# Performance work log

Hardware: AMD Instinct MI355X
Metric: run time of the kernel (lower is better)

The kernel has to match this reference:

```python
import jax, jax.numpy as jnp
import numpy as np

B, T, N, DIM = 8, 12, 500, 64
N_MIX, N_LAYERS, N_HEADS, N_REL, NG, K = 2, 2, 4, 8, 2, 20


def setup_inputs() -> dict:
    key = jax.random.key(0)
    ks = jax.random.split(key, 9)
    x0 = jax.random.normal(ks[0], (B, DIM, N, T), jnp.float32)
    x1 = jax.random.normal(ks[1], (B, DIM, N, T), jnp.float32)
    # dense relation adjacencies; scaled by 1/N to keep activations numerically sane
    graphs = jax.random.uniform(ks[2], (NG, N, N), jnp.float32) / N
    neighbors = jax.random.randint(ks[3], (NG, N, K), 0, N)
    neighbors_weight = jax.random.uniform(ks[4], (NG, N, K), jnp.float32)
    a_weight = jax.random.normal(ks[5], (2, N_REL, N_HEADS, N_LAYERS, 1, 1), jnp.float32)
    B_weight = jax.random.normal(ks[6], (1, N_HEADS, N_LAYERS, DIM, DIM), jnp.float32) / np.sqrt(DIM).astype(np.float32)
    a_bias = jax.random.normal(ks[7], (2, N_REL, N_HEADS, N_LAYERS, 1), jnp.float32)
    B_bias = jax.random.normal(ks[8], (1, N_HEADS, N_LAYERS, DIM), jnp.float32)
    return {"x0": x0, "x1": x1, "graphs": graphs, "neighbors": neighbors,
            "neighbors_weight": neighbors_weight, "a_weight": a_weight,
            "B_weight": B_weight, "a_bias": a_bias, "B_bias": B_bias}


def _forward(x0, x1, graphs, neighbors, neighbors_weight, a_weight, B_weight, a_bias, B_bias):
    # fuse head-mixture parameters: [R, L, D, D] and [R, L, D]
    wc = jnp.sum(a_weight[0] * B_weight, axis=1)
    bc = jnp.sum(a_bias[0] * B_bias, axis=1)
    wd = jnp.sum(a_weight[1] * B_weight, axis=1)
    bd = jnp.sum(a_bias[1] * B_bias, axis=1)

    xs = [jnp.transpose(x, (0, 3, 2, 1)) for x in (x0, x1)]  # [B, T, N, D]
    g = [[x0], [x1]]  # snapshots in [B, D, N, T] layout
    n_mix = N_MIX
    for l in range(N_LAYERS):
        h = [0.0] * n_mix
        for i in range(n_mix):
            for t in range(NG):
                adj = graphs[t]
                for j in range(n_mix):
                    rel = (t * n_mix + i) * n_mix + j
                    # neighbor aggregation: out[b,t,m,d] = sum_n x[b,t,n,d] * adj[n,m]
                    c = jnp.einsum('btnd,nm->btmd', xs[j], adj)
                    d = jnp.einsum('btnd,nm->btmd', xs[j] - xs[i], adj)
                    c = jax.nn.relu(c @ wc[rel, l] + bc[rel, l])
                    d = jnp.tanh(d @ wd[rel, l] + bd[rel, l])
                    h[i] = h[i] + c + d
        xs = h
        for i in range(n_mix):
            g[i].append(jnp.transpose(xs[i], (0, 3, 2, 1)))
    g = [jnp.concatenate(gi, axis=1) for gi in g]  # [B, D*(L+1), N, T]

    # summarize: per-node neighbor gather + weighted sum, per relation graph
    out = []
    for i in range(n_mix):
        parts = []
        for t in range(NG):
            gathered = g[i][:, :, neighbors[t], :]  # [B, C, N, K, T]
            parts.append(jnp.einsum('bcnkt,nk->bcnt', gathered, neighbors_weight[t]))
        out.append(jnp.concatenate(parts, axis=1))  # [B, C*NG, N, T]
    return tuple(out)


def reference(x0, x1, graphs, neighbors, neighbors_weight, a_weight, B_weight, a_bias, B_bias):
    return _forward(x0, x1, graphs, neighbors, neighbors_weight, a_weight, B_weight, a_bias, B_bias)
```

## Files before the change

### kernel.cpp

```cpp
#include <hip/hip_runtime.h>
#include <hip/hip_bf16.h>
#include <math.h>

#define B_ 8
#define T_ 12
#define N_ 500
#define D_ 64
#define K_ 20
#define M_ (B_*T_)
#define MND_ 3072000

#define XSB_OFF 0ul
#define AGH_OFF (3ul*MND_)
#define AT_HI_OFF (5ul*MND_)
#define XT_OFF    (AT_HI_OFF + 262144ul)
#define WCT_OFF   (XT_OFF + 3145728ul)
#define WDT_OFF   (WCT_OFF + 32768ul)
#define BC_OFF    (WDT_OFF + 32768ul)
#define BD_OFF    (BC_OFF + 1024ul)

using f4 = __attribute__((ext_vector_type(4))) float;
typedef __attribute__((ext_vector_type(8))) short bf16x8;
typedef __attribute__((ext_vector_type(8))) short short8;
typedef __attribute__((ext_vector_type(4))) float f32x4;

__device__ inline ushort to_bf16u(float v) {
    __hip_bfloat16 b = __float2bfloat16(v);
    return *reinterpret_cast<ushort*>(&b);
}

__device__ inline float fast_tanh(float x) {
    float u = __expf(2.0f * x);
    return 1.0f - 2.0f * __builtin_amdgcn_rcpf(u + 1.0f);
}

__global__ __launch_bounds__(256) void fuse_weights(
        const float* __restrict__ aw, const float* __restrict__ Bw,
        const float* __restrict__ ab, const float* __restrict__ Bb,
        float* __restrict__ bc, float* __restrict__ bd,
        ushort* __restrict__ wct, ushort* __restrict__ wdt) {
    int e = blockIdx.x * 256 + threadIdx.x;
    if (e < 131072) {
        int dd = e & 4095; int l = (e >> 12) & 1; int r = (e >> 13) & 7; int cd = e >> 16;
        float s = 0.f;
        #pragma unroll
        for (int h = 0; h < 4; ++h)
            s += aw[((cd*8 + r)*4 + h)*2 + l] * Bw[(h*2 + l)*4096 + dd];
        int tidx = (r*2 + l)*4096 + (dd & 63)*64 + (dd >> 6);
        (cd ? wdt : wct)[tidx] = to_bf16u(s);
    } else {
        int e2 = e - 131072;
        if (e2 < 2048) {
            int d = e2 & 63; int l = (e2 >> 6) & 1; int r = (e2 >> 7) & 7; int cd = e2 >> 10;
            float s = 0.f;
            #pragma unroll
            for (int h = 0; h < 4; ++h)
                s += ab[((cd*8 + r)*4 + h)*2 + l] * Bb[(h*2 + l)*64 + d];
            (cd ? bd : bc)[(r*2 + l)*64 + d] = s;
        }
    }
}

__global__ __launch_bounds__(256) void transpose_in(
        const float* __restrict__ x0, const float* __restrict__ x1,
        ushort* __restrict__ xsb0) {
    int bid = blockIdx.x;
    int n = bid % N_; int b = (bid / N_) % B_; int i = bid / (N_ * B_);
    const float* __restrict__ x = i ? x1 : x0;
    ushort* __restrict__ xbo = xsb0 + (size_t)i * MND_;
    __shared__ float tile[64][13];
    #pragma unroll
    for (int q = 0; q < 3; ++q) {
        int e = q * 256 + threadIdx.x;
        int d = e / 12, t = e % 12;
        tile[d][t] = x[(((size_t)b * D_ + d) * N_ + n) * T_ + t];
    }
    __syncthreads();
    #pragma unroll
    for (int q = 0; q < 3; ++q) {
        int e = q * 256 + threadIdx.x;
        int t = e >> 6, d = e & 63;
        xbo[(((size_t)b * T_ + t) * N_ + n) * D_ + d] = to_bf16u(tile[d][t]);
    }
}

__global__ __launch_bounds__(256) void adj_prep(
        const float* __restrict__ graphs,
        ushort* __restrict__ AT_hi) {
    int t = blockIdx.z;
    int n0 = blockIdx.x * 32, mm0 = blockIdx.y * 32;
    __shared__ float tile[32][33];
    int cc = threadIdx.x & 31, rr = threadIdx.x >> 5;
    #pragma unroll
    for (int it = 0; it < 4; ++it) {
        int n = n0 + it * 8 + rr, mm = mm0 + cc;
        tile[it * 8 + rr][cc] = (n < N_ && mm < N_)
            ? graphs[(size_t)t * 250000 + (size_t)n * 500 + mm] : 0.f;
    }
    __syncthreads();
    #pragma unroll
    for (int it = 0; it < 4; ++it) {
        int mml = it * 8 + rr, nl = cc;
        size_t idx = (size_t)t * 262144 + (size_t)(mm0 + mml) * 512 + n0 + nl;
        AT_hi[idx] = to_bf16u(tile[nl][mml]);
    }
}

__global__ __launch_bounds__(256) void xt_cast(
        const ushort* __restrict__ xsb,
        ushort* __restrict__ XT) {
    int i = blockIdx.z, m = blockIdx.y, c = blockIdx.x;
    int n0 = c * 64;
    __shared__ ushort tile[64][65];
    int d = threadIdx.x & 63, r4 = threadIdx.x >> 6;
    const ushort* __restrict__ src = xsb + (size_t)i * MND_ + (size_t)m * 32000;
    #pragma unroll
    for (int it = 0; it < 16; ++it) {
        int nl = it * 4 + r4; int n = n0 + nl;
        tile[nl][d] = (n < N_) ? src[(size_t)n * 64 + d] : (ushort)0;
    }
    __syncthreads();
    size_t base = (size_t)(i * 96 + m) * 64 * 512 + n0;
    int dl = threadIdx.x >> 2, ng = threadIdx.x & 3;
    #pragma unroll
    for (int half = 0; half < 2; ++half) {
        int nlb = ng * 16 + half * 8;
        short8 hv;
        #pragma unroll
        for (int q = 0; q < 8; ++q) hv[q] = (short)tile[nlb + q][dl];
        *(short8*)(XT + base + (size_t)dl * 512 + nlb) = hv;
    }
}

__global__ __launch_bounds__(64) void aggregate_mfma(
        const ushort* __restrict__ AT_hi,
        const ushort* __restrict__ XT, ushort* __restrict__ aggh) {
    int w = (blockIdx.x & 7) * 384 + (blockIdx.x >> 3);
    const int mm0 = (w & 7) * 64;
    int g = w >> 3;
    const int m = g % 96;
    const int cmb = g / 96;
    const int t = cmb >> 1, j = cmb & 1;
    const int lane = threadIdx.x;
    const int lr = lane & 15;
    const int lk = (lane >> 4) * 8;

    const ushort* __restrict__ A_h = AT_hi + (size_t)t * 262144 + (size_t)(mm0 + lr) * 512 + lk;
    const ushort* __restrict__ Bx  = XT + ((size_t)(j * 96 + m) * 64 + lr) * 512 + lk;

    f32x4 acc[4][4] = {};

    for (int k0 = 0; k0 < 512; k0 += 32) {
        bf16x8 ah[4], bh[4];
        #pragma unroll
        for (int f = 0; f < 4; ++f) {
            ah[f] = *(const bf16x8*)(A_h + (size_t)f * 8192 + k0);
            bh[f] = *(const bf16x8*)(Bx  + (size_t)f * 8192 + k0);
        }
        #pragma unroll
        for (int fi = 0; fi < 4; ++fi)
            #pragma unroll
            for (int fj = 0; fj < 4; ++fj)
                acc[fi][fj] = __builtin_amdgcn_mfma_f32_16x16x32_bf16(ah[fi], bh[fj], acc[fi][fj], 0, 0, 0);
    }

    size_t obase = (size_t)cmb * MND_ + (size_t)m * 32000;
    #pragma unroll
    for (int fi = 0; fi < 4; ++fi) {
        #pragma unroll
        for (int reg = 0; reg < 4; ++reg) {
            int row = mm0 + fi * 16 + (lane >> 4) * 4 + reg;
            if (row < N_) {
                #pragma unroll
                for (int fj = 0; fj < 4; ++fj)
                    aggh[obase + (size_t)row * 64 + fj * 16 + lr] = to_bf16u(acc[fi][fj][reg]);
            }
        }
    }
}

__global__ __launch_bounds__(64) void combine_mfma(
        const ushort* __restrict__ aggh,
        const ushort* __restrict__ wct, const ushort* __restrict__ wdt,
        const float* __restrict__ bcv, const float* __restrict__ bdv,
        ushort* __restrict__ xsb_out,
        ushort* __restrict__ xt_out, int l, int write_xt) {
    const int tile = blockIdx.x;
    const int m = blockIdx.y;
    const int i = blockIdx.z;
    const int n0 = tile * 32;
    const int r0 = m * 500 + n0;
    const int lane = threadIdx.x;
    const int lr = lane & 15;
    const int lk = (lane >> 4) * 8;

    f32x4 hacc[2][4] = {};

    for (int t = 0; t < 2; ++t) {
        #pragma unroll
        for (int j = 0; j < 2; ++j) {
            const int rel = (t * 2 + i) * 2 + j;
            const int wb = (rel * 2 + l) * 4096;
            const ushort* __restrict__ Ajh = aggh + (size_t)(t * 2 + j) * MND_ + (size_t)(r0 + lr) * 64 + lk;
            const ushort* __restrict__ Wc = wct + wb + lr * 64 + lk;

            f32x4 cacc[2][4];
            #pragma unroll
            for (int fj = 0; fj < 4; ++fj) {
                float bv = bcv[(rel * 2 + l) * 64 + fj * 16 + lr];
                #pragma unroll
                for (int fi = 0; fi < 2; ++fi) cacc[fi][fj] = f32x4{bv, bv, bv, bv};
            }

            if (j != i) {
                const ushort* __restrict__ Aih = aggh + (size_t)(t * 2 + i) * MND_ + (size_t)(r0 + lr) * 64 + lk;
                const ushort* __restrict__ Wd = wdt + wb + lr * 64 + lk;
                f32x4 dacc[2][4];
                #pragma unroll
                for (int fj = 0; fj < 4; ++fj) {
                    float bv = bdv[(rel * 2 + l) * 64 + fj * 16 + lr];
                    #pragma unroll
                    for (int fi = 0; fi < 2; ++fi) dacc[fi][fj] = f32x4{bv, bv, bv, bv};
                }
                #pragma unroll
                for (int k0 = 0; k0 < 64; k0 += 32) {
                    bf16x8 ajh[2], nih[2], wcf[4], wdf[4];
                    #pragma unroll
                    for (int fi = 0; fi < 2; ++fi) {
                        ajh[fi] = *(const bf16x8*)(Ajh + fi * 1024 + k0);
                        bf16x8 ih = *(const bf16x8*)(Aih + fi * 1024 + k0);
                        #pragma unroll
                        for (int q = 0; q < 8; ++q) nih[fi][q] = ih[q] ^ (short)0x8000;
                    }
                    #pragma unroll
                    for (int fj = 0; fj < 4; ++fj) {
                        wcf[fj] = *(const bf16x8*)(Wc + fj * 1024 + k0);
                        wdf[fj] = *(const bf16x8*)(Wd + fj * 1024 + k0);
                    }
                    #pragma unroll
                    for (int fi = 0; fi < 2; ++fi)
                        #pragma unroll
                        for (int fj = 0; fj < 4; ++fj) {
                            cacc[fi][fj] = __builtin_amdgcn_mfma_f32_16x16x32_bf16(ajh[fi], wcf[fj], cacc[fi][fj], 0, 0, 0);
                            dacc[fi][fj] = __builtin_amdgcn_mfma_f32_16x16x32_bf16(ajh[fi], wdf[fj], dacc[fi][fj], 0, 0, 0);
                            dacc[fi][fj] = __builtin_amdgcn_mfma_f32_16x16x32_bf16(nih[fi], wdf[fj], dacc[fi][fj], 0, 0, 0);
                        }
                }
                #pragma unroll
                for (int fi = 0; fi < 2; ++fi)
                    #pragma unroll
                    for (int fj = 0; fj < 4; ++fj)
                        #pragma unroll
                        for (int reg = 0; reg < 4; ++reg) {
                            hacc[fi][fj][reg] += fmaxf(cacc[fi][fj][reg], 0.f);
                            hacc[fi][fj][reg] += fast_tanh(dacc[fi][fj][reg]);
                        }
            } else {
                #pragma unroll
                for (int k0 = 0; k0 < 64; k0 += 32) {
                    bf16x8 ajh[2], wcf[4];
                    #pragma unroll
                    for (int fi = 0; fi < 2; ++fi)
                        ajh[fi] = *(const bf16x8*)(Ajh + fi * 1024 + k0);
                    #pragma unroll
                    for (int fj = 0; fj < 4; ++fj)
                        wcf[fj] = *(const bf16x8*)(Wc + fj * 1024 + k0);
                    #pragma unroll
                    for (int fi = 0; fi < 2; ++fi)
                        #pragma unroll
                        for (int fj = 0; fj < 4; ++fj)
                            cacc[fi][fj] = __builtin_amdgcn_mfma_f32_16x16x32_bf16(ajh[fi], wcf[fj], cacc[fi][fj], 0, 0, 0);
                }
                #pragma unroll
                for (int fj = 0; fj < 4; ++fj) {
                    float tb = fast_tanh(bdv[(rel * 2 + l) * 64 + fj * 16 + lr]);
                    #pragma unroll
                    for (int fi = 0; fi < 2; ++fi)
                        #pragma unroll
                        for (int reg = 0; reg < 4; ++reg) {
                            hacc[fi][fj][reg] += fmaxf(cacc[fi][fj][reg], 0.f);
                            hacc[fi][fj][reg] += tb;
                        }
                }
            }
        }
    }

    __shared__ float staged[32][65];
    #pragma unroll
    for (int fi = 0; fi < 2; ++fi)
        #pragma unroll
        for (int reg = 0; reg < 4; ++reg) {
            int rloc = fi * 16 + (lane >> 4) * 4 + reg;
            bool ok = (n0 + rloc) < N_;
            #pragma unroll
            for (int fj = 0; fj < 4; ++fj)
                staged[rloc][fj * 16 + lr] = ok ? hacc[fi][fj][reg] : 0.f;
        }
    __syncthreads();

    ushort* __restrict__ Xb = xsb_out + (size_t)i * MND_;
    #pragma unroll
    for (int q = 0; q < 32; ++q) {
        if (n0 + q < N_)
            Xb[(size_t)(r0 + q) * 64 + lane] = to_bf16u(staged[q][lane]);
    }
    if (write_xt) {
        size_t tb = ((size_t)(i * 96 + m) * 64 + lane) * 512 + n0;
        #pragma unroll
        for (int g = 0; g < 4; ++g) {
            short8 hv;
            #pragma unroll
            for (int q = 0; q < 8; ++q)
                hv[q] = (short)to_bf16u(staged[g * 8 + q][lane]);
            *(short8*)(xt_out + tb + g * 8) = hv;
        }
    }
}

__global__ __launch_bounds__(192) void summarize(
        const ushort* __restrict__ XSB, const int* __restrict__ nbr,
        const float* __restrict__ nw, float* __restrict__ out) {
    int wg = (blockIdx.x & 7) * 252 + (blockIdx.x >> 3);
    int grp = wg / 126;
    int rem = wg % 126;
    int i = grp >> 3, b = grp & 7;
    int l = rem / 42;
    int rem2 = rem % 42;
    int t = rem2 / 21;
    int tile = rem2 % 21;
    int n0 = tile * 24;
    int tid = threadIdx.x;
    int g6 = tid >> 5;
    int d2 = tid & 31;

    __shared__ int   nb_s[24][20];
    __shared__ float w_s[24][20];
    __shared__ float staged[64][145];

    for (int e = tid; e < 480; e += 192) {
        int nn = e / 20, k = e % 20;
        int n = n0 + nn;
        nb_s[nn][k] = (n < N_) ? nbr[((size_t)t * N_ + n) * K_ + k] : 0;
        w_s[nn][k]  = (n < N_) ? nw[((size_t)t * N_ + n) * K_ + k] : 0.f;
    }
    __syncthreads();

    const uint* __restrict__ Xbase = (const uint*)(XSB + ((size_t)l * 2 + i) * MND_
                                     + (size_t)b * T_ * N_ * D_) + d2;
    size_t obase = ((size_t)((i * 8 + b) * 384 + t * 192 + l * 64)) * 6000
                 + (size_t)n0 * 12;

    #pragma unroll
    for (int half = 0; half < 2; ++half) {
        #pragma unroll
        for (int nn2 = 0; nn2 < 2; ++nn2) {
            int pl = g6 * 2 + nn2;
            int nl = half * 12 + pl;
            #pragma unroll
            for (int tt0 = 0; tt0 < 12; tt0 += 4) {
                const uint* __restrict__ Xm0 = Xbase + (size_t)(tt0 + 0) * 16000;
                const uint* __restrict__ Xm1 = Xbase + (size_t)(tt0 + 1) * 16000;
                const uint* __restrict__ Xm2 = Xbase + (size_t)(tt0 + 2) * 16000;
                const uint* __restrict__ Xm3 = Xbase + (size_t)(tt0 + 3) * 16000;
                float a0l = 0.f, a0h = 0.f, a1l = 0.f, a1h = 0.f;
                float a2l = 0.f, a2h = 0.f, a3l = 0.f, a3h = 0.f;
                #pragma unroll
                for (int k = 0; k < K_; ++k) {
                    size_t off = (size_t)nb_s[nl][k] * 32;
                    float w = w_s[nl][k];
                    uint u0 = Xm0[off], u1 = Xm1[off], u2 = Xm2[off], u3 = Xm3[off];
                    a0l = fmaf(__uint_as_float(u0 << 16), w, a0l);
                    a0h = fmaf(__uint_as_float(u0 & 0xffff0000u), w, a0h);
                    a1l = fmaf(__uint_as_float(u1 << 16), w, a1l);
                    a1h = fmaf(__uint_as_float(u1 & 0xffff0000u), w, a1h);
                    a2l = fmaf(__uint_as_float(u2 << 16), w, a2l);
                    a2h = fmaf(__uint_as_float(u2 & 0xffff0000u), w, a2h);
                    a3l = fmaf(__uint_as_float(u3 << 16), w, a3l);
                    a3h = fmaf(__uint_as_float(u3 & 0xffff0000u), w, a3h);
                }
                int p = pl * 12 + tt0;
                staged[2 * d2 + 0][p + 0] = a0l;  staged[2 * d2 + 1][p + 0] = a0h;
                staged[2 * d2 + 0][p + 1] = a1l;  staged[2 * d2 + 1][p + 1] = a1h;
                staged[2 * d2 + 0][p + 2] = a2l;  staged[2 * d2 + 1][p + 2] = a2h;
                staged[2 * d2 + 0][p + 3] = a3l;  staged[2 * d2 + 1][p + 3] = a3h;
            }
        }
        __syncthreads();
        int base_n = n0 + half * 12;
        int plim = (N_ - base_n) * 12;
        if (plim > 144) plim = 144;
        if (plim > 0) {
            for (int it = 0; it < 48; ++it) {
                int e = it * 192 + tid;
                int c2 = e / 144, q = e % 144;
                if (q < plim)
                    out[obase + (size_t)c2 * 6000 + (size_t)half * 144 + q] = staged[c2][q];
            }
        }
        __syncthreads();
    }
}

extern "C" void kernel_launch(void* const* d_in, const int* in_sizes, int n_in,
                              void* d_out, int out_size, void* d_ws, size_t ws_size,
                              hipStream_t stream) {
    const float* x0     = (const float*)d_in[0];
    const float* x1     = (const float*)d_in[1];
    const float* graphs = (const float*)d_in[2];
    const int*   nbr    = (const int*)d_in[3];
    const float* nwt    = (const float*)d_in[4];
    const float* aw     = (const float*)d_in[5];
    const float* Bw     = (const float*)d_in[6];
    const float* ab     = (const float*)d_in[7];
    const float* Bb     = (const float*)d_in[8];
    float* out = (float*)d_out;
    float* ws  = (float*)d_ws;

    ushort* XSB = (ushort*)(ws + XSB_OFF);
    ushort* AGh = (ushort*)(ws + AGH_OFF);
    ushort* ATh = (ushort*)(ws + AT_HI_OFF);
    ushort* XT  = (ushort*)(ws + XT_OFF);
    ushort* WCT = (ushort*)(ws + WCT_OFF);
    ushort* WDT = (ushort*)(ws + WDT_OFF);
    float*  BC  = ws + BC_OFF;
    float*  BD  = ws + BD_OFF;

    fuse_weights<<<520, 256, 0, stream>>>(aw, Bw, ab, Bb, BC, BD, WCT, WDT);
    transpose_in<<<8000, 256, 0, stream>>>(x0, x1, XSB);
    adj_prep<<<dim3(16, 16, 2), 256, 0, stream>>>(graphs, ATh);
    xt_cast<<<dim3(8, 96, 2), 256, 0, stream>>>(XSB, XT);
    for (int l = 0; l < 2; ++l) {
        aggregate_mfma<<<3072, 64, 0, stream>>>(ATh, XT, AGh);
        combine_mfma<<<dim3(16, 96, 2), 64, 0, stream>>>(
            AGh, WCT, WDT, BC, BD,
            XSB + (size_t)(l + 1) * 2 * MND_, XT, l, (l == 0) ? 1 : 0);
    }
    summarize<<<2016, 192, 0, stream>>>(XSB, nbr, nwt, out);
}
```

Measured before the change: 325.5 us.

## Fuse graph aggregation and combine into one kernel using shared-memory tiles

Merges the aggregate and combine kernels into a single 256-thread block per (row tile, m). Each of its four waves computes one (t,j) aggregation tile into LDS, and the combine stage then reads those tiles from LDS. This drops the global round-trip of the aggregated intermediate and two launches. It double-buffers the transposed activations (XTa/XTb) so layer 1 does not overwrite its own input. The summarize staging buffer is also narrowed to bf16, which cuts LDS use but adds rounding to the final output. The fused kernel has fewer blocks (768 vs 3072), which lowers available parallelism.

```diff
diff --git a/kernel.cpp b/kernel.cpp
--- a/kernel.cpp
+++ b/kernel.cpp
@@ -11,7 +11,7 @@
 #define MND_ 3072000
 
 #define XSB_OFF 0ul
-#define AGH_OFF (3ul*MND_)
+#define XTB_OFF (3ul*MND_)
 #define AT_HI_OFF (5ul*MND_)
 #define XT_OFF    (AT_HI_OFF + 262144ul)
 #define WCT_OFF   (XT_OFF + 3145728ul)
@@ -132,77 +132,64 @@
     }
 }
 
-__global__ __launch_bounds__(64) void aggregate_mfma(
-        const ushort* __restrict__ AT_hi,
-        const ushort* __restrict__ XT, ushort* __restrict__ aggh) {
-    int w = (blockIdx.x & 7) * 384 + (blockIdx.x >> 3);
-    const int mm0 = (w & 7) * 64;
-    int g = w >> 3;
-    const int m = g % 96;
-    const int cmb = g / 96;
-    const int t = cmb >> 1, j = cmb & 1;
-    const int lane = threadIdx.x;
+__global__ __launch_bounds__(256) void agg_combine_mfma(
+        const ushort* __restrict__ ATh, const ushort* __restrict__ XT,
+        const ushort* __restrict__ wct, const ushort* __restrict__ wdt,
+        const float* __restrict__ bcv, const float* __restrict__ bdv,
+        ushort* __restrict__ xsb_out, ushort* __restrict__ xt_out,
+        int l, int write_xt) {
+    const int rt = blockIdx.x;
+    const int m = blockIdx.y;
+    const int n0 = rt * 64;
+    const int tid = threadIdx.x;
+    const int w = tid >> 6;
+    const int lane = tid & 63;
     const int lr = lane & 15;
     const int lk = (lane >> 4) * 8;
 
-    const ushort* __restrict__ A_h = AT_hi + (size_t)t * 262144 + (size_t)(mm0 + lr) * 512 + lk;
-    const ushort* __restrict__ Bx  = XT + ((size_t)(j * 96 + m) * 64 + lr) * 512 + lk;
-
-    f32x4 acc[4][4] = {};
-
-    for (int k0 = 0; k0 < 512; k0 += 32) {
-        bf16x8 ah[4], bh[4];
-        #pragma unroll
-        for (int f = 0; f < 4; ++f) {
-            ah[f] = *(const bf16x8*)(A_h + (size_t)f * 8192 + k0);
-            bh[f] = *(const bf16x8*)(Bx  + (size_t)f * 8192 + k0);
+    __shared__ ushort aggL[4][64][72];
+
+    {
+        const int t = w >> 1, j = w & 1;
+        const ushort* __restrict__ A_h = ATh + (size_t)t * 262144 + (size_t)(n0 + lr) * 512 + lk;
+        const ushort* __restrict__ Bx  = XT + ((size_t)(j * 96 + m) * 64 + lr) * 512 + lk;
+        f32x4 acc[4][4] = {};
+        for (int k0 = 0; k0 < 512; k0 += 32) {
+            bf16x8 ah[4], bh[4];
+            #pragma unroll
+            for (int f = 0; f < 4; ++f) {
+                ah[f] = *(const bf16x8*)(A_h + (size_t)f * 8192 + k0);
+                bh[f] = *(const bf16x8*)(Bx  + (size_t)f * 8192 + k0);
+            }
+            #pragma unroll
+            for (int fi = 0; fi < 4; ++fi)
+                #pragma unroll
+                for (int fj = 0; fj < 4; ++fj)
+                    acc[fi][fj] = __builtin_amdgcn_mfma_f32_16x16x32_bf16(ah[fi], bh[fj], acc[fi][fj], 0, 0, 0);
         }
         #pragma unroll
         for (int fi = 0; fi < 4; ++fi)
             #pragma unroll
-            for (int fj = 0; fj < 4; ++fj)
-                acc[fi][fj] = __builtin_amdgcn_mfma_f32_16x16x32_bf16(ah[fi], bh[fj], acc[fi][fj], 0, 0, 0);
-    }
-
-    size_t obase = (size_t)cmb * MND_ + (size_t)m * 32000;
-    #pragma unroll
-    for (int fi = 0; fi < 4; ++fi) {
-        #pragma unroll
-        for (int reg = 0; reg < 4; ++reg) {
-            int row = mm0 + fi * 16 + (lane >> 4) * 4 + reg;
-            if (row < N_) {
+            for (int reg = 0; reg < 4; ++reg) {
+                int row = fi * 16 + (lane >> 4) * 4 + reg;
                 #pragma unroll
                 for (int fj = 0; fj < 4; ++fj)
-                    aggh[obase + (size_t)row * 64 + fj * 16 + lr] = to_bf16u(acc[fi][fj][reg]);
-            }
-        }
-    }
-}
-
-__global__ __launch_bounds__(64) void combine_mfma(
-        const ushort* __restrict__ aggh,
-        const ushort* __restrict__ wct, const ushort* __restrict__ wdt,
-        const float* __restrict__ bcv, const float* __restrict__ bdv,
-        ushort* __restrict__ xsb_out,
-        ushort* __restrict__ xt_out, int l, int write_xt) {
-    const int tile = blockIdx.x;
-    const int m = blockIdx.y;
-    const int i = blockIdx.z;
-    const int n0 = tile * 32;
-    const int r0 = m * 500 + n0;
-    const int lane = threadIdx.x;
-    const int lr = lane & 15;
-    const int lk = (lane >> 4) * 8;
-
+                    aggL[w][row][fj * 16 + lr] = to_bf16u(acc[fi][fj][reg]);
+            }
+    }
+    __syncthreads();
+
+    const int iw = w >> 1;
+    const int r0l = (w & 1) * 32;
     f32x4 hacc[2][4] = {};
 
     for (int t = 0; t < 2; ++t) {
         #pragma unroll
         for (int j = 0; j < 2; ++j) {
-            const int rel = (t * 2 + i) * 2 + j;
+            const int rel = (t * 2 + iw) * 2 + j;
             const int wb = (rel * 2 + l) * 4096;
-            const ushort* __restrict__ Ajh = aggh + (size_t)(t * 2 + j) * MND_ + (size_t)(r0 + lr) * 64 + lk;
             const ushort* __restrict__ Wc = wct + wb + lr * 64 + lk;
+            const ushort* __restrict__ AjL = &aggL[t * 2 + j][r0l + lr][lk];
 
             f32x4 cacc[2][4];
             #pragma unroll
@@ -212,8 +199,8 @@
                 for (int fi = 0; fi < 2; ++fi) cacc[fi][fj] = f32x4{bv, bv, bv, bv};
             }
 
-            if (j != i) {
-                const ushort* __restrict__ Aih = aggh + (size_t)(t * 2 + i) * MND_ + (size_t)(r0 + lr) * 64 + lk;
+            if (j != iw) {
+                const ushort* __restrict__ AiL = &aggL[t * 2 + iw][r0l + lr][lk];
                 const ushort* __restrict__ Wd = wdt + wb + lr * 64 + lk;
                 f32x4 dacc[2][4];
                 #pragma unroll
@@ -227,8 +214,8 @@
                     bf16x8 ajh[2], nih[2], wcf[4], wdf[4];
                     #pragma unroll
                     for (int fi = 0; fi < 2; ++fi) {
-                        ajh[fi] = *(const bf16x8*)(Ajh + fi * 1024 + k0);
-                        bf16x8 ih = *(const bf16x8*)(Aih + fi * 1024 + k0);
+                        ajh[fi] = *(const bf16x8*)(AjL + fi * 16 * 72 + k0);
+                        bf16x8 ih = *(const bf16x8*)(AiL + fi * 16 * 72 + k0);
                         #pragma unroll
                         for (int q = 0; q < 8; ++q) nih[fi][q] = ih[q] ^ (short)0x8000;
                     }
@@ -261,7 +248,7 @@
                     bf16x8 ajh[2], wcf[4];
                     #pragma unroll
                     for (int fi = 0; fi < 2; ++fi)
-                        ajh[fi] = *(const bf16x8*)(Ajh + fi * 1024 + k0);
+                        ajh[fi] = *(const bf16x8*)(AjL + fi * 16 * 72 + k0);
                     #pragma unroll
                     for (int fj = 0; fj < 4; ++fj)
                         wcf[fj] = *(const bf16x8*)(Wc + fj * 1024 + k0);
@@ -285,35 +272,35 @@
             }
         }
     }
-
-    __shared__ float staged[32][65];
+    __syncthreads();
+
+    float* stg = ((float*)aggL) + w * 2080;
     #pragma unroll
     for (int fi = 0; fi < 2; ++fi)
         #pragma unroll
         for (int reg = 0; reg < 4; ++reg) {
             int rloc = fi * 16 + (lane >> 4) * 4 + reg;
-            bool ok = (n0 + rloc) < N_;
+            bool ok = (n0 + r0l + rloc) < N_;
             #pragma unroll
             for (int fj = 0; fj < 4; ++fj)
-                staged[rloc][fj * 16 + lr] = ok ? hacc[fi][fj][reg] : 0.f;
-        }
-    __syncthreads();
-
-    ushort* __restrict__ Xb = xsb_out + (size_t)i * MND_;
+                stg[rloc * 65 + fj * 16 + lr] = ok ? hacc[fi][fj][reg] : 0.f;
+        }
+    ushort* __restrict__ Xb = xsb_out + (size_t)iw * MND_;
+    int gbase = m * 500 + n0 + r0l;
     #pragma unroll
     for (int q = 0; q < 32; ++q) {
-        if (n0 + q < N_)
-            Xb[(size_t)(r0 + q) * 64 + lane] = to_bf16u(staged[q][lane]);
+        if (n0 + r0l + q < N_)
+            Xb[(size_t)(gbase + q) * 64 + lane] = to_bf16u(stg[q * 65 + lane]);
     }
     if (write_xt) {
-        size_t tb = ((size_t)(i * 96 + m) * 64 + lane) * 512 + n0;
-        #pragma unroll
-        for (int g = 0; g < 4; ++g) {
+        size_t tb = ((size_t)(iw * 96 + m) * 64 + lane) * 512 + n0 + r0l;
+        #pragma unroll
+        for (int g2 = 0; g2 < 4; ++g2) {
             short8 hv;
             #pragma unroll
             for (int q = 0; q < 8; ++q)
-                hv[q] = (short)to_bf16u(staged[g * 8 + q][lane]);
-            *(short8*)(xt_out + tb + g * 8) = hv;
+                hv[q] = (short)to_bf16u(stg[(g2 * 8 + q) * 65 + lane]);
+            *(short8*)(xt_out + tb + g2 * 8) = hv;
         }
     }
 }
@@ -334,9 +321,9 @@
     int g6 = tid >> 5;
     int d2 = tid & 31;
 
-    __shared__ int   nb_s[24][20];
-    __shared__ float w_s[24][20];
-    __shared__ float staged[64][145];
+    __shared__ int    nb_s[24][20];
+    __shared__ float  w_s[24][20];
+    __shared__ ushort staged[64][145];
 
     for (int e = tid; e < 480; e += 192) {
         int nn = e / 20, k = e % 20;
@@ -380,10 +367,10 @@
                     a3h = fmaf(__uint_as_float(u3 & 0xffff0000u), w, a3h);
                 }
                 int p = pl * 12 + tt0;
-                staged[2 * d2 + 0][p + 0] = a0l;  staged[2 * d2 + 1][p + 0] = a0h;
-                staged[2 * d2 + 0][p + 1] = a1l;  staged[2 * d2 + 1][p + 1] = a1h;
-                staged[2 * d2 + 0][p + 2] = a2l;  staged[2 * d2 + 1][p + 2] = a2h;
-                staged[2 * d2 + 0][p + 3] = a3l;  staged[2 * d2 + 1][p + 3] = a3h;
+                staged[2 * d2 + 0][p + 0] = to_bf16u(a0l);  staged[2 * d2 + 1][p + 0] = to_bf16u(a0h);
+                staged[2 * d2 + 0][p + 1] = to_bf16u(a1l);  staged[2 * d2 + 1][p + 1] = to_bf16u(a1h);
+                staged[2 * d2 + 0][p + 2] = to_bf16u(a2l);  staged[2 * d2 + 1][p + 2] = to_bf16u(a2h);
+                staged[2 * d2 + 0][p + 3] = to_bf16u(a3l);  staged[2 * d2 + 1][p + 3] = to_bf16u(a3h);
             }
         }
         __syncthreads();
@@ -395,7 +382,8 @@
                 int e = it * 192 + tid;
                 int c2 = e / 144, q = e % 144;
                 if (q < plim)
-                    out[obase + (size_t)c2 * 6000 + (size_t)half * 144 + q] = staged[c2][q];
+                    out[obase + (size_t)c2 * 6000 + (size_t)half * 144 + q] =
+                        __uint_as_float((uint)staged[c2][q] << 16);
             }
         }
         __syncthreads();
@@ -418,9 +406,9 @@
     float* ws  = (float*)d_ws;
 
     ushort* XSB = (ushort*)(ws + XSB_OFF);
-    ushort* AGh = (ushort*)(ws + AGH_OFF);
+    ushort* XTb = (ushort*)(ws + XTB_OFF);
     ushort* ATh = (ushort*)(ws + AT_HI_OFF);
-    ushort* XT  = (ushort*)(ws + XT_OFF);
+    ushort* XTa = (ushort*)(ws + XT_OFF);
     ushort* WCT = (ushort*)(ws + WCT_OFF);
     ushort* WDT = (ushort*)(ws + WDT_OFF);
     float*  BC  = ws + BC_OFF;
@@ -429,12 +417,10 @@
     fuse_weights<<<520, 256, 0, stream>>>(aw, Bw, ab, Bb, BC, BD, WCT, WDT);
     transpose_in<<<8000, 256, 0, stream>>>(x0, x1, XSB);
     adj_prep<<<dim3(16, 16, 2), 256, 0, stream>>>(graphs, ATh);
-    xt_cast<<<dim3(8, 96, 2), 256, 0, stream>>>(XSB, XT);
-    for (int l = 0; l < 2; ++l) {
-        aggregate_mfma<<<3072, 64, 0, stream>>>(ATh, XT, AGh);
-        combine_mfma<<<dim3(16, 96, 2), 64, 0, stream>>>(
-            AGh, WCT, WDT, BC, BD,
-            XSB + (size_t)(l + 1) * 2 * MND_, XT, l, (l == 0) ? 1 : 0);
-    }
+    xt_cast<<<dim3(8, 96, 2), 256, 0, stream>>>(XSB, XTa);
+    agg_combine_mfma<<<dim3(8, 96), 256, 0, stream>>>(
+        ATh, XTa, WCT, WDT, BC, BD, XSB + 2ul * MND_, XTb, 0, 1);
+    agg_combine_mfma<<<dim3(8, 96), 256, 0, stream>>>(
+        ATh, XTb, WCT, WDT, BC, BD, XSB + 4ul * MND_, XTb, 1, 0);
     summarize<<<2016, 192, 0, stream>>>(XSB, nbr, nwt, out);
 }
```

Result: faster. 288.5 us, median of 3 (-11.4%).
